# Kernel optimization log

Hardware: AMD Instinct MI355X
Metric: run time of the kernel (lower is better)

Reference implementation:

```python
import jax, jax.numpy as jnp
import numpy as np

N, C, LM, ELEMS = 1024, 128, 16, 10   # nodes, channels, lm components (lmax=3), elements
P1, P2, P3 = 4, 12, 30                # generalized-CG path counts per correlation order
DIMS = (1, 3)                         # output irreps kept: 0e (dim 1), 1o (dim 3)


def _sparse(rng, shape, density=0.15):
    # stand-in generalized Clebsch-Gordan U tensor: fixed, sparse constants
    a = rng.standard_normal(shape).astype(np.float32)
    return jnp.asarray(a * (rng.random(shape) < density))


def setup_inputs() -> dict:
    k = jax.random.split(jax.random.key(0), 2)
    rng = np.random.default_rng(0)
    inp = {
        'x': jax.random.normal(k[0], (N, C, LM), jnp.float32),
        'species': jax.random.randint(k[1], (N,), 0, ELEMS, jnp.int32),
    }
    for i, d in enumerate(DIMS):
        inp[f'U1_{i}'] = _sparse(rng, (d, LM, P1))
        inp[f'U2_{i}'] = _sparse(rng, (d, LM, LM, P2))
        inp[f'U3_{i}'] = _sparse(rng, (d, LM, LM, LM, P3))
        for nu, p in ((1, P1), (2, P2), (3, P3)):
            inp[f'W{nu}_{i}'] = jnp.asarray((rng.standard_normal((ELEMS, p, C)) / np.sqrt(p)).astype(np.float32))
        inp[f'Wlin_{i}'] = jnp.asarray(rng.standard_normal((C, C)).astype(np.float32))
    return inp


def _sym_contract(x, species, U1, U2, U3, W1, W2, W3):
    # MACE recursive symmetric contraction, highest correlation order first.
    # x: [n, c, m] (channels factored to separate axis); species selects per-element weights.
    out = jnp.einsum('Lijmp,npc,ncm->ncLij', U3, W3[species], x)          # nu = 3 term
    out = jnp.einsum('Lijp,npc->ncLij', U2, W2[species]) + out            # add nu = 2 basis
    out = jnp.einsum('ncLij,ncj->ncLi', out, x)                           # contract one power of x
    out = jnp.einsum('Lip,npc->ncLi', U1, W1[species]) + out              # add nu = 1 basis
    return jnp.einsum('ncLi,nci->ncL', out, x)                            # [n, c, dim_L]


def _forward(x, species, U1_0, U2_0, U3_0, W1_0, W2_0, W3_0, Wlin_0,
             U1_1, U2_1, U3_1, W1_1, W2_1, W3_1, Wlin_1):
    f0 = _sym_contract(x, species, U1_0, U2_0, U3_0, W1_0, W2_0, W3_0)    # [n, C, 1]
    f1 = _sym_contract(x, species, U1_1, U2_1, U3_1, W1_1, W2_1, W3_1)    # [n, C, 3]
    s = 1.0 / float(np.sqrt(C))                                            # e3nn.Linear path norm
    y0 = jnp.einsum('nc,ck->nk', f0[..., 0], Wlin_0) * s                  # 128x0e block
    y1 = jnp.einsum('nci,ck->nki', f1, Wlin_1) * s                        # 128x1o block
    return jnp.concatenate([y0, y1.reshape(y1.shape[0], -1)], axis=-1)    # [n, 128 + 384]


def reference(x, species, U1_0, U2_0, U3_0, W1_0, W2_0, W3_0, Wlin_0,
              U1_1, U2_1, U3_1, W1_1, W2_1, W3_1, Wlin_1):
    return _forward(x, species, U1_0, U2_0, U3_0, W1_0, W2_0, W3_0, Wlin_0,
                    U1_1, U2_1, U3_1, W1_1, W2_1, W3_1, Wlin_1)
```

## Files before the change

kernel.cpp:

```cpp
#include <hip/hip_runtime.h>
#include <hip/hip_fp16.h>

typedef float v2f __attribute__((ext_vector_type(2)));

#define NN    1024
#define CC    128
#define NELEM 10
#define NQ3   816
#define NQ2   136
#define NQ    968
#define KP    48
#define QT    11
#define NTILE 88

#define NL_OFF    0
#define CNT_OFF   40960
#define CALL_OFF  524288
#define UHAT_OFF  10485760
#define F_OFF     20447232

__device__ __constant__ int d_OFF2[16] = {0,16,31,45,58,70,81,91,100,108,115,121,126,130,133,135};
__device__ __constant__ int d_OFF3[16] = {0,136,256,361,452,530,596,651,696,732,760,781,796,806,812,815};

__global__ void k_setup(const float* __restrict__ U3_0, const float* __restrict__ U3_1,
                        const float* __restrict__ U2_0, const float* __restrict__ U2_1,
                        const float* __restrict__ U1_0, const float* __restrict__ U1_1,
                        const int* __restrict__ species,
                        float* __restrict__ uhat, int* __restrict__ nodelist,
                        int* __restrict__ counts) {
    if (blockIdx.x < 64) {
        int tid = blockIdx.x * 256 + threadIdx.x;
        int Lout = tid >> 12;
        int r = tid & 4095;
        int a = r >> 8, b = (r >> 4) & 15, m = r & 15;
        if (a > b || b > m) return;
        int q = d_OFF3[a] + (d_OFF2[b] - d_OFF2[a]) + (m - b);
        const float* U = (Lout == 0) ? U3_0 : U3_1;
        int L = (Lout == 0) ? 0 : (Lout - 1);
        int P[6][3] = {{a,b,m},{a,m,b},{b,a,m},{b,m,a},{m,a,b},{m,b,a}};
        float s[30];
#pragma unroll
        for (int p = 0; p < 30; ++p) s[p] = 0.f;
        for (int t = 0; t < 6; ++t) {
            bool dup = false;
            for (int u = 0; u < t; ++u)
                if (P[u][0] == P[t][0] && P[u][1] == P[t][1] && P[u][2] == P[t][2]) dup = true;
            if (dup) continue;
            const float* src = U + ((((L * 16 + P[t][0]) * 16 + P[t][1]) * 16 + P[t][2]) * 30);
#pragma unroll
            for (int p = 0; p < 30; ++p) s[p] += src[p];
        }
        float* dst = uhat + ((size_t)Lout * NQ + q) * KP;
#pragma unroll
        for (int p = 0; p < 30; ++p) dst[p] = s[p];
#pragma unroll
        for (int p = 30; p < KP; ++p) dst[p] = 0.f;
    } else if (blockIdx.x < 69) {
        int tid = (blockIdx.x - 64) * 256 + threadIdx.x;
        if (tid < 1024) {
            int Lout = tid >> 8;
            int r = tid & 255;
            int a = r >> 4, b = r & 15;
            if (a > b) return;
            int q = NQ3 + d_OFF2[a] + (b - a);
            const float* U = (Lout == 0) ? U2_0 : U2_1;
            int L = (Lout == 0) ? 0 : (Lout - 1);
            float* dst = uhat + ((size_t)Lout * NQ + q) * KP;
#pragma unroll
            for (int p = 0; p < 30; ++p) dst[p] = 0.f;
#pragma unroll
            for (int p = 0; p < 12; ++p) {
                float v = U[((L * 16 + a) * 16 + b) * 12 + p];
                if (a != b) v += U[((L * 16 + b) * 16 + a) * 12 + p];
                dst[30 + p] = v;
            }
#pragma unroll
            for (int p = 42; p < KP; ++p) dst[p] = 0.f;
        } else if (tid < 1024 + 64) {
            int s2 = tid - 1024;
            int Lout = s2 >> 4, i = s2 & 15;
            int q = NQ3 + NQ2 + i;
            const float* U = (Lout == 0) ? U1_0 : U1_1;
            int L = (Lout == 0) ? 0 : (Lout - 1);
            float* dst = uhat + ((size_t)Lout * NQ + q) * KP;
#pragma unroll
            for (int p = 0; p < 42; ++p) dst[p] = 0.f;
#pragma unroll
            for (int p = 0; p < 4; ++p) dst[42 + p] = U[(L * 16 + i) * 4 + p];
            dst[46] = 0.f; dst[47] = 0.f;
        }
    } else {
        __shared__ int cnt[NELEM];
        int t = threadIdx.x;
        if (t < NELEM) cnt[t] = 0;
        __syncthreads();
#pragma unroll
        for (int j = 0; j < 4; ++j) {
            int node = t * 4 + j;
            int e = species[node];
            int pos = atomicAdd(&cnt[e], 1);
            nodelist[e * NN + pos] = node;
        }
        __syncthreads();
        if (t < NELEM) counts[t] = cnt[t];
    }
}

__global__ __launch_bounds__(256) void k_fold(
    const float* __restrict__ uhat,
    const float* __restrict__ W1_0, const float* __restrict__ W2_0, const float* __restrict__ W3_0,
    const float* __restrict__ W1_1, const float* __restrict__ W2_1, const float* __restrict__ W3_1,
    uint2* __restrict__ call4h) {
    __shared__ __align__(16) float uh_lds[4][QT][KP];
    int e  = blockIdx.x / NTILE;
    int qt = blockIdx.x % NTILE;
    int t = threadIdx.x;
    {
        const float4* src4 = (const float4*)uhat;
        float4* dst4 = (float4*)uh_lds;
        for (int i = t; i < 4 * QT * 12; i += 256) {
            int l = i / (QT * 12);
            int r = i - l * (QT * 12);
            int qloc = r / 12, p4 = r % 12;
            dst4[i] = src4[((size_t)l * NQ + qt * QT + qloc) * 12 + p4];
        }
    }
    int c  = t & 127;
    int qs = t >> 7;
    float wr[2][KP];
#pragma unroll
    for (int p = 0; p < 30; ++p) {
        wr[0][p] = W3_0[(e * 30 + p) * CC + c];
        wr[1][p] = W3_1[(e * 30 + p) * CC + c];
    }
#pragma unroll
    for (int p = 0; p < 12; ++p) {
        wr[0][30 + p] = W2_0[(e * 12 + p) * CC + c];
        wr[1][30 + p] = W2_1[(e * 12 + p) * CC + c];
    }
#pragma unroll
    for (int p = 0; p < 4; ++p) {
        wr[0][42 + p] = W1_0[(e * 4 + p) * CC + c];
        wr[1][42 + p] = W1_1[(e * 4 + p) * CC + c];
    }
    wr[0][46] = wr[0][47] = wr[1][46] = wr[1][47] = 0.f;
    __syncthreads();
    size_t base = ((size_t)e * CC + c) * NQ;
    for (int j = 0; j < 6; ++j) {
        int qloc = qs * 6 + j;
        if (qloc >= QT) break;
        int q = qt * QT + qloc;
        float r[4];
#pragma unroll
        for (int l = 0; l < 4; ++l) {
            const float4* up = (const float4*)uh_lds[l][qloc];
            const float* w = (l == 0) ? wr[0] : wr[1];
            float acc0 = 0.f, acc1 = 0.f, acc2 = 0.f, acc3 = 0.f;
#pragma unroll
            for (int p4 = 0; p4 < 12; ++p4) {
                float4 u = up[p4];
                acc0 = fmaf(u.x, w[p4 * 4 + 0], acc0);
                acc1 = fmaf(u.y, w[p4 * 4 + 1], acc1);
                acc2 = fmaf(u.z, w[p4 * 4 + 2], acc2);
                acc3 = fmaf(u.w, w[p4 * 4 + 3], acc3);
            }
            r[l] = (acc0 + acc1) + (acc2 + acc3);
        }
        __half2 h01 = __floats2half2_rn(r[0], r[1]);
        __half2 h23 = __floats2half2_rn(r[2], r[3]);
        uint2 v;
        v.x = *(unsigned int*)&h01;
        v.y = *(unsigned int*)&h23;
        call4h[base + q] = v;
    }
}

#define CUBIC(A0, A1) { \
    _Pragma("unroll") for (int a = (A0); a < (A1); ++a) { \
        _Pragma("unroll") for (int b = a; b < 16; ++b) { \
            v2f pab = xv[a] * xv[b]; \
            _Pragma("unroll") for (int m = b; m < 16; ++m) { \
                float4 w = cf_lds[q]; v2f mo = pab * xv[m]; \
                a0 += mo * w.x; a1 += mo * w.y; a2 += mo * w.z; a3 += mo * w.w; ++q; } } } }

#define QUAD(A0, A1) { \
    _Pragma("unroll") for (int a = (A0); a < (A1); ++a) { \
        _Pragma("unroll") for (int b = a; b < 16; ++b) { \
            float4 w = cf_lds[q]; v2f mo = xv[a] * xv[b]; \
            a0 += mo * w.x; a1 += mo * w.y; a2 += mo * w.z; a3 += mo * w.w; ++q; } } }

__global__ __launch_bounds__(256, 4) void k_eval(
    const float* __restrict__ x, const int* __restrict__ nodelist,
    const int* __restrict__ counts, const uint2* __restrict__ call4h,
    float4* __restrict__ fout) {
    __shared__ __align__(16) float4 cf_lds[NQ];
    __shared__ __align__(16) v2f part[3][64][4];
    int ec = blockIdx.x;
    int e = ec >> 7;
    int c = ec & 127;
    int cnt = counts[e];
    const uint2* src = call4h + (size_t)ec * NQ;
    int t = threadIdx.x;
    for (int i = t; i < NQ; i += 256) {
        uint2 pk = src[i];
        __half2 h01 = *(__half2*)&pk.x, h23 = *(__half2*)&pk.y;
        cf_lds[i] = make_float4(__half2float(h01.x), __half2float(h01.y),
                                __half2float(h23.x), __half2float(h23.y));
    }
    __syncthreads();
    int slice = t >> 6;
    int lane  = t & 63;

    for (int sb = 0; sb < cnt; sb += 128) {
        int i0 = sb + lane * 2, i1 = i0 + 1;
        bool v0i = i0 < cnt, v1i = i1 < cnt;
        int n0 = v0i ? nodelist[e * NN + i0] : 0;
        int n1 = v1i ? nodelist[e * NN + i1] : 0;
        const float4* xp0 = (const float4*)(x + ((size_t)n0 * CC + c) * 16);
        const float4* xp1 = (const float4*)(x + ((size_t)n1 * CC + c) * 16);
        float4 p0 = xp0[0], p1 = xp0[1], p2 = xp0[2], p3 = xp0[3];
        float4 q0 = xp1[0], q1 = xp1[1], q2 = xp1[2], q3 = xp1[3];
        v2f xv[16];
        xv[0]  = v2f{p0.x, q0.x}; xv[1]  = v2f{p0.y, q0.y};
        xv[2]  = v2f{p0.z, q0.z}; xv[3]  = v2f{p0.w, q0.w};
        xv[4]  = v2f{p1.x, q1.x}; xv[5]  = v2f{p1.y, q1.y};
        xv[6]  = v2f{p1.z, q1.z}; xv[7]  = v2f{p1.w, q1.w};
        xv[8]  = v2f{p2.x, q2.x}; xv[9]  = v2f{p2.y, q2.y};
        xv[10] = v2f{p2.z, q2.z}; xv[11] = v2f{p2.w, q2.w};
        xv[12] = v2f{p3.x, q3.x}; xv[13] = v2f{p3.y, q3.y};
        xv[14] = v2f{p3.z, q3.z}; xv[15] = v2f{p3.w, q3.w};
        if (!v0i) {
#pragma unroll
            for (int m = 0; m < 16; ++m) xv[m].x = 0.f;
        }
        if (!v1i) {
#pragma unroll
            for (int m = 0; m < 16; ++m) xv[m].y = 0.f;
        }
        v2f a0 = {0.f, 0.f}, a1 = {0.f, 0.f}, a2 = {0.f, 0.f}, a3 = {0.f, 0.f};
        int q;
        if (slice == 0) {
            q = 0;   CUBIC(0, 2);
        } else if (slice == 1) {
            q = 256; CUBIC(2, 4);
            q = NQ3; QUAD(0, 4);
        } else if (slice == 2) {
            q = 452; CUBIC(4, 7);
            q = NQ3 + 58; QUAD(4, 10);
        } else {
            q = 651; CUBIC(7, 16);
            q = NQ3 + 115; QUAD(10, 16);
            q = NQ3 + NQ2;
#pragma unroll
            for (int a = 0; a < 16; ++a) {
                float4 w = cf_lds[q]; v2f mo = xv[a];
                a0 += mo * w.x; a1 += mo * w.y; a2 += mo * w.z; a3 += mo * w.w; ++q;
            }
        }
        if (slice > 0) {
            part[slice - 1][lane][0] = a0; part[slice - 1][lane][1] = a1;
            part[slice - 1][lane][2] = a2; part[slice - 1][lane][3] = a3;
        }
        __syncthreads();
        if (slice == 0) {
            v2f s0 = a0 + part[0][lane][0] + part[1][lane][0] + part[2][lane][0];
            v2f s1 = a1 + part[0][lane][1] + part[1][lane][1] + part[2][lane][1];
            v2f s2 = a2 + part[0][lane][2] + part[1][lane][2] + part[2][lane][2];
            v2f s3 = a3 + part[0][lane][3] + part[1][lane][3] + part[2][lane][3];
            if (v0i) fout[(size_t)n0 * CC + c] = make_float4(s0.x, s1.x, s2.x, s3.x);
            if (v1i) fout[(size_t)n1 * CC + c] = make_float4(s0.y, s1.y, s2.y, s3.y);
        }
        __syncthreads();
    }
}

__global__ __launch_bounds__(256) void k_linear(
    const float4* __restrict__ fin, const float* __restrict__ Wlin0,
    const float* __restrict__ Wlin1, float* __restrict__ out) {
    __shared__ float4 fl[512];
    int t = threadIdx.x;
    fl[t]       = fin[(size_t)blockIdx.x * 512 + t];
    fl[t + 256] = fin[(size_t)blockIdx.x * 512 + t + 256];
    __syncthreads();
    int nh = t >> 7, k = t & 127;
    int n = blockIdx.x * 4 + nh * 2;
    float a0 = 0.f, a1 = 0.f, a2 = 0.f, a3 = 0.f;
    float b0 = 0.f, b1 = 0.f, b2 = 0.f, b3 = 0.f;
#pragma unroll 8
    for (int c = 0; c < CC; ++c) {
        float4 f0 = fl[(nh * 2) * CC + c];
        float4 f1 = fl[(nh * 2 + 1) * CC + c];
        float w0 = Wlin0[c * CC + k];
        float w1 = Wlin1[c * CC + k];
        a0 = fmaf(f0.x, w0, a0); a1 = fmaf(f0.y, w1, a1);
        a2 = fmaf(f0.z, w1, a2); a3 = fmaf(f0.w, w1, a3);
        b0 = fmaf(f1.x, w0, b0); b1 = fmaf(f1.y, w1, b1);
        b2 = fmaf(f1.z, w1, b2); b3 = fmaf(f1.w, w1, b3);
    }
    const float s = 0.08838834764831845f;
    float* o = out + (size_t)n * 512;
    o[k] = a0 * s;
    o[128 + 3 * k + 0] = a1 * s;
    o[128 + 3 * k + 1] = a2 * s;
    o[128 + 3 * k + 2] = a3 * s;
    o += 512;
    o[k] = b0 * s;
    o[128 + 3 * k + 0] = b1 * s;
    o[128 + 3 * k + 1] = b2 * s;
    o[128 + 3 * k + 2] = b3 * s;
}

extern "C" void kernel_launch(void* const* d_in, const int* in_sizes, int n_in,
                              void* d_out, int out_size, void* d_ws, size_t ws_size,
                              hipStream_t stream) {
    const float* x     = (const float*)d_in[0];
    const int*   spec  = (const int*)d_in[1];
    const float* U1_0  = (const float*)d_in[2];
    const float* U2_0  = (const float*)d_in[3];
    const float* U3_0  = (const float*)d_in[4];
    const float* W1_0  = (const float*)d_in[5];
    const float* W2_0  = (const float*)d_in[6];
    const float* W3_0  = (const float*)d_in[7];
    const float* Wl_0  = (const float*)d_in[8];
    const float* U1_1  = (const float*)d_in[9];
    const float* U2_1  = (const float*)d_in[10];
    const float* U3_1  = (const float*)d_in[11];
    const float* W1_1  = (const float*)d_in[12];
    const float* W2_1  = (const float*)d_in[13];
    const float* W3_1  = (const float*)d_in[14];
    const float* Wl_1  = (const float*)d_in[15];

    char* ws = (char*)d_ws;
    int*    nodelist = (int*)(ws + NL_OFF);
    int*    counts   = (int*)(ws + CNT_OFF);
    uint2*  call4h   = (uint2*)(ws + CALL_OFF);
    float*  uhat     = (float*)(ws + UHAT_OFF);
    float4* fbuf     = (float4*)(ws + F_OFF);

    k_setup<<<dim3(70), dim3(256), 0, stream>>>(U3_0, U3_1, U2_0, U2_1, U1_0, U1_1,
                                                spec, uhat, nodelist, counts);
    k_fold<<<dim3(880), dim3(256), 0, stream>>>(uhat, W1_0, W2_0, W3_0,
                                                W1_1, W2_1, W3_1, call4h);
    k_eval<<<dim3(1280), dim3(256), 0, stream>>>(x, nodelist, counts, call4h, fbuf);
    k_linear<<<dim3(256), dim3(256), 0, stream>>>(fbuf, Wl_0, Wl_1, (float*)d_out);
}
```

Baseline: 83.32 us.

## Keep contraction coefficients as fp16 in LDS with padded pair-aligned layout

```diff
diff --git a/kernel.cpp b/kernel.cpp
--- a/kernel.cpp
+++ b/kernel.cpp
@@ -13,10 +13,54 @@
 #define QT    11
 #define NTILE 88
 
+constexpr int rnd2c(int s) { return (s + 1) & ~1; }
+constexpr int cub_start(int A, int B) {
+    int s = 0;
+    for (int a = 0; a < 16; ++a)
+        for (int b = a; b < 16; ++b) {
+            s = rnd2c(s);
+            if (a == A && b == B) return s;
+            s += 16 - b;
+        }
+    return rnd2c(s);
+}
+constexpr int quad_start(int A) {
+    int s = cub_start(16, 0);
+    for (int a = 0; a < 16; ++a) {
+        s = rnd2c(s);
+        if (a == A) return s;
+        s += 16 - a;
+    }
+    return rnd2c(s);
+}
+constexpr int LIN_START = quad_start(16);
+constexpr int NSLOT = (LIN_START + 16 + 1) & ~1;
+static_assert(cub_start(0, 0) == 0, "layout");
+static_assert(NSLOT <= 1152, "lds budget");
+
+struct SlotTab {
+    unsigned short t[NQ];
+    constexpr SlotTab() : t{} {
+        int q = 0, s = 0;
+        for (int a = 0; a < 16; ++a)
+            for (int b = a; b < 16; ++b) {
+                s = rnd2c(s);
+                for (int m = b; m < 16; ++m) t[q++] = (unsigned short)(s++);
+            }
+        for (int a = 0; a < 16; ++a) {
+            s = rnd2c(s);
+            for (int b = a; b < 16; ++b) t[q++] = (unsigned short)(s++);
+        }
+        s = rnd2c(s);
+        for (int i = 0; i < 16; ++i) t[q++] = (unsigned short)(s++);
+    }
+};
+__device__ __constant__ SlotTab kSlot = SlotTab();
+
 #define NL_OFF    0
 #define CNT_OFF   40960
 #define CALL_OFF  524288
-#define UHAT_OFF  10485760
+#define UHAT_OFF  12582912
 #define F_OFF     20447232
 
 __device__ __constant__ int d_OFF2[16] = {0,16,31,45,58,70,81,91,100,108,115,121,126,130,133,135};
@@ -145,7 +189,7 @@
     }
     wr[0][46] = wr[0][47] = wr[1][46] = wr[1][47] = 0.f;
     __syncthreads();
-    size_t base = ((size_t)e * CC + c) * NQ;
+    size_t base = ((size_t)e * CC + c) * NSLOT;
     for (int j = 0; j < 6; ++j) {
         int qloc = qs * 6 + j;
         if (qloc >= QT) break;
@@ -171,55 +215,82 @@
         uint2 v;
         v.x = *(unsigned int*)&h01;
         v.y = *(unsigned int*)&h23;
-        call4h[base + q] = v;
-    }
-}
+        call4h[base + kSlot.t[q]] = v;
+    }
+}
+
+#define PAIR_FMA(MO1, MO2) { \
+    uint4 pk4 = *(const uint4*)(cf16 + q); \
+    __half2 ha = *(__half2*)&pk4.x, hb = *(__half2*)&pk4.y; \
+    __half2 hc = *(__half2*)&pk4.z, hd = *(__half2*)&pk4.w; \
+    v2f mo1 = (MO1), mo2 = (MO2); \
+    a0 += mo1 * __half2float(ha.x); a1 += mo1 * __half2float(ha.y); \
+    a2 += mo1 * __half2float(hb.x); a3 += mo1 * __half2float(hb.y); \
+    a0 += mo2 * __half2float(hc.x); a1 += mo2 * __half2float(hc.y); \
+    a2 += mo2 * __half2float(hd.x); a3 += mo2 * __half2float(hd.y); \
+    q += 2; }
+
+#define ONE_FMA(MO) { \
+    uint2 pk2 = *(const uint2*)(cf16 + q); \
+    __half2 ha = *(__half2*)&pk2.x, hb = *(__half2*)&pk2.y; \
+    v2f mo = (MO); \
+    a0 += mo * __half2float(ha.x); a1 += mo * __half2float(ha.y); \
+    a2 += mo * __half2float(hb.x); a3 += mo * __half2float(hb.y); \
+    q += 1; }
 
 #define CUBIC(A0, A1) { \
     _Pragma("unroll") for (int a = (A0); a < (A1); ++a) { \
         _Pragma("unroll") for (int b = a; b < 16; ++b) { \
+            q = (q + 1) & ~1; \
             v2f pab = xv[a] * xv[b]; \
-            _Pragma("unroll") for (int m = b; m < 16; ++m) { \
-                float4 w = cf_lds[q]; v2f mo = pab * xv[m]; \
-                a0 += mo * w.x; a1 += mo * w.y; a2 += mo * w.z; a3 += mo * w.w; ++q; } } } }
+            int m = b; \
+            _Pragma("unroll") for (; m + 1 < 16; m += 2) PAIR_FMA(pab * xv[m], pab * xv[m + 1]); \
+            if (m < 16) ONE_FMA(pab * xv[m]); \
+        } } }
 
 #define QUAD(A0, A1) { \
     _Pragma("unroll") for (int a = (A0); a < (A1); ++a) { \
-        _Pragma("unroll") for (int b = a; b < 16; ++b) { \
-            float4 w = cf_lds[q]; v2f mo = xv[a] * xv[b]; \
-            a0 += mo * w.x; a1 += mo * w.y; a2 += mo * w.z; a3 += mo * w.w; ++q; } } }
-
-__global__ __launch_bounds__(256, 4) void k_eval(
+        q = (q + 1) & ~1; \
+        int b = a; \
+        _Pragma("unroll") for (; b + 1 < 16; b += 2) PAIR_FMA(xv[a] * xv[b], xv[a] * xv[b + 1]); \
+        if (b < 16) ONE_FMA(xv[a] * xv[b]); \
+    } }
+
+__global__ __launch_bounds__(256, 3) void k_eval(
     const float* __restrict__ x, const int* __restrict__ nodelist,
     const int* __restrict__ counts, const uint2* __restrict__ call4h,
     float4* __restrict__ fout) {
-    __shared__ __align__(16) float4 cf_lds[NQ];
+    __shared__ __align__(16) uint2 cf16[NSLOT];
     __shared__ __align__(16) v2f part[3][64][4];
     int ec = blockIdx.x;
     int e = ec >> 7;
     int c = ec & 127;
     int cnt = counts[e];
-    const uint2* src = call4h + (size_t)ec * NQ;
+    const uint2* src = call4h + (size_t)ec * NSLOT;
     int t = threadIdx.x;
-    for (int i = t; i < NQ; i += 256) {
-        uint2 pk = src[i];
-        __half2 h01 = *(__half2*)&pk.x, h23 = *(__half2*)&pk.y;
-        cf_lds[i] = make_float4(__half2float(h01.x), __half2float(h01.y),
-                                __half2float(h23.x), __half2float(h23.y));
-    }
-    __syncthreads();
     int slice = t >> 6;
     int lane  = t & 63;
 
+    int i0 = lane * 2, i1 = i0 + 1;
+    bool v0i = i0 < cnt, v1i = i1 < cnt;
+    int n0 = v0i ? nodelist[e * NN + i0] : 0;
+    int n1 = v1i ? nodelist[e * NN + i1] : 0;
+
+    for (int i = t; i < NSLOT / 2; i += 256)
+        ((uint4*)cf16)[i] = ((const uint4*)src)[i];
+
     for (int sb = 0; sb < cnt; sb += 128) {
-        int i0 = sb + lane * 2, i1 = i0 + 1;
-        bool v0i = i0 < cnt, v1i = i1 < cnt;
-        int n0 = v0i ? nodelist[e * NN + i0] : 0;
-        int n1 = v1i ? nodelist[e * NN + i1] : 0;
+        if (sb > 0) {
+            i0 = sb + lane * 2; i1 = i0 + 1;
+            v0i = i0 < cnt; v1i = i1 < cnt;
+            n0 = v0i ? nodelist[e * NN + i0] : 0;
+            n1 = v1i ? nodelist[e * NN + i1] : 0;
+        }
         const float4* xp0 = (const float4*)(x + ((size_t)n0 * CC + c) * 16);
         const float4* xp1 = (const float4*)(x + ((size_t)n1 * CC + c) * 16);
         float4 p0 = xp0[0], p1 = xp0[1], p2 = xp0[2], p3 = xp0[3];
         float4 q0 = xp1[0], q1 = xp1[1], q2 = xp1[2], q3 = xp1[3];
+        if (sb == 0) __syncthreads();
         v2f xv[16];
         xv[0]  = v2f{p0.x, q0.x}; xv[1]  = v2f{p0.y, q0.y};
         xv[2]  = v2f{p0.z, q0.z}; xv[3]  = v2f{p0.w, q0.w};
@@ -240,22 +311,19 @@
         v2f a0 = {0.f, 0.f}, a1 = {0.f, 0.f}, a2 = {0.f, 0.f}, a3 = {0.f, 0.f};
         int q;
         if (slice == 0) {
-            q = 0;   CUBIC(0, 2);
+            q = cub_start(0, 0); CUBIC(0, 2);
         } else if (slice == 1) {
-            q = 256; CUBIC(2, 4);
-            q = NQ3; QUAD(0, 4);
+            q = cub_start(2, 2); CUBIC(2, 4);
+            q = quad_start(0);   QUAD(0, 4);
         } else if (slice == 2) {
-            q = 452; CUBIC(4, 7);
-            q = NQ3 + 58; QUAD(4, 10);
+            q = cub_start(4, 4); CUBIC(4, 7);
+            q = quad_start(4);   QUAD(4, 10);
         } else {
-            q = 651; CUBIC(7, 16);
-            q = NQ3 + 115; QUAD(10, 16);
-            q = NQ3 + NQ2;
-#pragma unroll
-            for (int a = 0; a < 16; ++a) {
-                float4 w = cf_lds[q]; v2f mo = xv[a];
-                a0 += mo * w.x; a1 += mo * w.y; a2 += mo * w.z; a3 += mo * w.w; ++q;
-            }
+            q = cub_start(7, 7); CUBIC(7, 16);
+            q = quad_start(10);  QUAD(10, 16);
+            q = LIN_START;
+#pragma unroll
+            for (int a = 0; a < 16; a += 2) PAIR_FMA(xv[a], xv[a + 1]);
         }
         if (slice > 0) {
             part[slice - 1][lane][0] = a0; part[slice - 1][lane][1] = a1;
```

Result: faster. 75.13 us (-9.8%).

## Give each wavefront a whole (element,channel) pair and drop cross-slice reduction

Applied to the files above, without the earlier changes.

```diff
diff --git a/kernel.cpp b/kernel.cpp
--- a/kernel.cpp
+++ b/kernel.cpp
@@ -175,41 +175,40 @@
     }
 }
 
+#define COEF(W0, W1, W2, W3) \
+    uint2 pk = cf[q]; \
+    __half2 h01 = *(__half2*)&pk.x; __half2 h23 = *(__half2*)&pk.y; \
+    float W0 = __half2float(h01.x), W1 = __half2float(h01.y); \
+    float W2 = __half2float(h23.x), W3 = __half2float(h23.y);
+
 #define CUBIC(A0, A1) { \
     _Pragma("unroll") for (int a = (A0); a < (A1); ++a) { \
         _Pragma("unroll") for (int b = a; b < 16; ++b) { \
             v2f pab = xv[a] * xv[b]; \
             _Pragma("unroll") for (int m = b; m < 16; ++m) { \
-                float4 w = cf_lds[q]; v2f mo = pab * xv[m]; \
-                a0 += mo * w.x; a1 += mo * w.y; a2 += mo * w.z; a3 += mo * w.w; ++q; } } } }
+                COEF(wx, wy, wz, ww); v2f mo = pab * xv[m]; \
+                a0 += mo * wx; a1 += mo * wy; a2 += mo * wz; a3 += mo * ww; ++q; } } } }
 
 #define QUAD(A0, A1) { \
     _Pragma("unroll") for (int a = (A0); a < (A1); ++a) { \
         _Pragma("unroll") for (int b = a; b < 16; ++b) { \
-            float4 w = cf_lds[q]; v2f mo = xv[a] * xv[b]; \
-            a0 += mo * w.x; a1 += mo * w.y; a2 += mo * w.z; a3 += mo * w.w; ++q; } } }
-
-__global__ __launch_bounds__(256, 4) void k_eval(
+            COEF(wx, wy, wz, ww); v2f mo = xv[a] * xv[b]; \
+            a0 += mo * wx; a1 += mo * wy; a2 += mo * wz; a3 += mo * ww; ++q; } } }
+
+__global__ __launch_bounds__(128, 2) void k_eval(
     const float* __restrict__ x, const int* __restrict__ nodelist,
     const int* __restrict__ counts, const uint2* __restrict__ call4h,
     float4* __restrict__ fout) {
-    __shared__ __align__(16) float4 cf_lds[NQ];
-    __shared__ __align__(16) v2f part[3][64][4];
-    int ec = blockIdx.x;
-    int e = ec >> 7;
-    int c = ec & 127;
+    __shared__ __align__(16) uint2 cf16[2][NQ];
+    int t = threadIdx.x;
+    int widx = t >> 6, lane = t & 63;
+    int ec = blockIdx.x * 2 + widx;
+    int e = ec >> 7, c = ec & 127;
     int cnt = counts[e];
     const uint2* src = call4h + (size_t)ec * NQ;
-    int t = threadIdx.x;
-    for (int i = t; i < NQ; i += 256) {
-        uint2 pk = src[i];
-        __half2 h01 = *(__half2*)&pk.x, h23 = *(__half2*)&pk.y;
-        cf_lds[i] = make_float4(__half2float(h01.x), __half2float(h01.y),
-                                __half2float(h23.x), __half2float(h23.y));
-    }
-    __syncthreads();
-    int slice = t >> 6;
-    int lane  = t & 63;
+    uint2* cf = cf16[widx];
+
+    for (int i = lane; i < NQ; i += 64) cf[i] = src[i];
 
     for (int sb = 0; sb < cnt; sb += 128) {
         int i0 = sb + lane * 2, i1 = i0 + 1;
@@ -238,39 +237,16 @@
             for (int m = 0; m < 16; ++m) xv[m].y = 0.f;
         }
         v2f a0 = {0.f, 0.f}, a1 = {0.f, 0.f}, a2 = {0.f, 0.f}, a3 = {0.f, 0.f};
-        int q;
-        if (slice == 0) {
-            q = 0;   CUBIC(0, 2);
-        } else if (slice == 1) {
-            q = 256; CUBIC(2, 4);
-            q = NQ3; QUAD(0, 4);
-        } else if (slice == 2) {
-            q = 452; CUBIC(4, 7);
-            q = NQ3 + 58; QUAD(4, 10);
-        } else {
-            q = 651; CUBIC(7, 16);
-            q = NQ3 + 115; QUAD(10, 16);
-            q = NQ3 + NQ2;
-#pragma unroll
-            for (int a = 0; a < 16; ++a) {
-                float4 w = cf_lds[q]; v2f mo = xv[a];
-                a0 += mo * w.x; a1 += mo * w.y; a2 += mo * w.z; a3 += mo * w.w; ++q;
-            }
-        }
-        if (slice > 0) {
-            part[slice - 1][lane][0] = a0; part[slice - 1][lane][1] = a1;
-            part[slice - 1][lane][2] = a2; part[slice - 1][lane][3] = a3;
-        }
-        __syncthreads();
-        if (slice == 0) {
-            v2f s0 = a0 + part[0][lane][0] + part[1][lane][0] + part[2][lane][0];
-            v2f s1 = a1 + part[0][lane][1] + part[1][lane][1] + part[2][lane][1];
-            v2f s2 = a2 + part[0][lane][2] + part[1][lane][2] + part[2][lane][2];
-            v2f s3 = a3 + part[0][lane][3] + part[1][lane][3] + part[2][lane][3];
-            if (v0i) fout[(size_t)n0 * CC + c] = make_float4(s0.x, s1.x, s2.x, s3.x);
-            if (v1i) fout[(size_t)n1 * CC + c] = make_float4(s0.y, s1.y, s2.y, s3.y);
-        }
-        __syncthreads();
+        int q = 0;
+        CUBIC(0, 16);
+        QUAD(0, 16);
+#pragma unroll
+        for (int a = 0; a < 16; ++a) {
+            COEF(wx, wy, wz, ww); v2f mo = xv[a];
+            a0 += mo * wx; a1 += mo * wy; a2 += mo * wz; a3 += mo * ww; ++q;
+        }
+        if (v0i) fout[(size_t)n0 * CC + c] = make_float4(a0.x, a1.x, a2.x, a3.x);
+        if (v1i) fout[(size_t)n1 * CC + c] = make_float4(a0.y, a1.y, a2.y, a3.y);
     }
 }
 
@@ -341,6 +317,6 @@
                                                 spec, uhat, nodelist, counts);
     k_fold<<<dim3(880), dim3(256), 0, stream>>>(uhat, W1_0, W2_0, W3_0,
                                                 W1_1, W2_1, W3_1, call4h);
-    k_eval<<<dim3(1280), dim3(256), 0, stream>>>(x, nodelist, counts, call4h, fbuf);
+    k_eval<<<dim3(640), dim3(128), 0, stream>>>(x, nodelist, counts, call4h, fbuf);
     k_linear<<<dim3(256), dim3(256), 0, stream>>>(fbuf, Wl_0, Wl_1, (float*)d_out);
 }
```

Result: slower. 259.8 us (+211.9%).
